# Performance work log

Measured on AMD Instinct MI355X. Metric: run time of the kernel, lower is better.

Reference implementation:

```python
import jax, jax.numpy as jnp
import numpy as np

N = 50000        # nodes
E = 800000       # edges
D = 64           # embedding_dim
N_GCN = 30       # stacked GCNConv layers
N_GGC = 8        # GatedGraphConv propagation steps


def setup_inputs() -> dict:
    key = jax.random.key(0)
    ks = jax.random.split(key, 12)
    s = 0.1
    x = jax.random.normal(ks[0], (N, 2 * D), dtype=jnp.float32)
    edge_index = jax.random.randint(ks[1], (2, E), 0, N, dtype=jnp.int32)
    return {
        "x": x,
        "edge_index": edge_index,
        "linear_w": jax.random.normal(ks[2], (D, 2 * D), dtype=jnp.float32) * s,
        "linear_b": jax.random.normal(ks[3], (D,), dtype=jnp.float32) * s,
        "gcn_w": jax.random.normal(ks[4], (N_GCN, D, D), dtype=jnp.float32) * s,
        "gcn_b": jax.random.normal(ks[5], (N_GCN, D), dtype=jnp.float32) * s,
        "ggc_w": jax.random.normal(ks[6], (N_GGC, D, D), dtype=jnp.float32) * s,
        "gru_w_ih": jax.random.normal(ks[7], (3 * D, D), dtype=jnp.float32) * s,
        "gru_w_hh": jax.random.normal(ks[8], (3 * D, D), dtype=jnp.float32) * s,
        "gru_b_ih": jax.random.normal(ks[9], (3 * D,), dtype=jnp.float32) * s,
        "gru_b_hh": jax.random.normal(ks[10], (3 * D,), dtype=jnp.float32) * s,
    }


def reference(x, edge_index, linear_w, linear_b, gcn_w, gcn_b,
              ggc_w, gru_w_ih, gru_w_hh, gru_b_ih, gru_b_hh):
    src, dst = edge_index[0], edge_index[1]

    # --- GCN normalization (self-loops added, symmetric deg^-1/2 norm) ---
    loop = jnp.arange(N, dtype=edge_index.dtype)
    src_sl = jnp.concatenate([src, loop])   # [E+N]
    dst_sl = jnp.concatenate([dst, loop])
    deg = jax.ops.segment_sum(jnp.ones(E + N, dtype=x.dtype), dst_sl, num_segments=N)
    dinv = deg ** -0.5                       # deg >= 1 because of self-loops
    norm = (dinv[src_sl] * dinv[dst_sl])[:, None]  # [E+N, 1]

    # --- initial linear + relu ---
    h = jax.nn.relu(x @ linear_w.T + linear_b)      # [N, D]

    # --- 30 stacked GCNConv layers (NOTE: original's in-loop relu is a no-op) ---
    def gcn_step(h, wb):
        W, b = wb
        xw = h @ W.T                                 # [N, D]
        msg = xw[src_sl] * norm                      # [E+N, D] gather
        out = jax.ops.segment_sum(msg, dst_sl, num_segments=N) + b
        return out, None

    h, _ = jax.lax.scan(gcn_step, h, (gcn_w, gcn_b))

    # --- GatedGraphConv(D, num_layers=8): add-aggregation + GRUCell ---
    def ggc_step(h, W):
        m = jax.ops.segment_sum((h @ W)[src], dst, num_segments=N)  # [N, D]
        gi = m @ gru_w_ih.T + gru_b_ih              # [N, 3D]
        gh = h @ gru_w_hh.T + gru_b_hh
        ir, iz, inn = jnp.split(gi, 3, axis=1)
        hr, hz, hn = jnp.split(gh, 3, axis=1)
        r = jax.nn.sigmoid(ir + hr)
        z = jax.nn.sigmoid(iz + hz)
        n = jnp.tanh(inn + r * hn)
        h_new = (1.0 - z) * n + z * h
        return h_new, None

    h, _ = jax.lax.scan(ggc_step, h, ggc_w)
    # l2 / gate / cross_graph in the original are dead code; only h is returned
    return h
```

## Files before the change

### kernel.cpp

```cpp
#include <hip/hip_runtime.h>
#include <math.h>

#define NN 50000
#define NE 800000
#define DD 64
#define N_GCN 30
#define N_GGC 8
#define NB ((NN + 255) / 256)
#define NPB 6

__device__ __forceinline__ float lane_bcast(float v, int k) {
    return __int_as_float(__builtin_amdgcn_readlane(__float_as_int(v), k));
}


__global__ void hist_kernel(const int* __restrict__ dst, int* __restrict__ cnt) {
    int i = blockIdx.x * blockDim.x + threadIdx.x;
    if (i < NE) atomicAdd(&cnt[dst[i]], 1);
}

__global__ void dinv_kernel(const int* __restrict__ cnt, float* __restrict__ dinv) {
    int i = blockIdx.x * blockDim.x + threadIdx.x;
    if (i < NN) dinv[i] = rsqrtf((float)cnt[i] + 1.0f);
}

__global__ void scan1_kernel(const int* __restrict__ cnt, int* __restrict__ bsum) {
    __shared__ int s[256];
    int tid = threadIdx.x;
    int i = blockIdx.x * 256 + tid;
    s[tid] = (i < NN) ? cnt[i] : 0;
    __syncthreads();
    for (int off = 128; off > 0; off >>= 1) {
        if (tid < off) s[tid] += s[tid + off];
        __syncthreads();
    }
    if (tid == 0) bsum[blockIdx.x] = s[0];
}

__global__ void scan2_kernel(int* __restrict__ bsum) {
    if (threadIdx.x == 0 && blockIdx.x == 0) {
        int acc = 0;
        for (int b = 0; b < NB; b++) { int v = bsum[b]; bsum[b] = acc; acc += v; }
        bsum[NB] = acc;
    }
}

__global__ void scan3_kernel(const int* __restrict__ cnt, const int* __restrict__ bsum,
                             int* __restrict__ rowptr) {
    __shared__ int s[256];
    int tid = threadIdx.x;
    int i = blockIdx.x * 256 + tid;
    int v = (i < NN) ? cnt[i] : 0;
    s[tid] = v;
    __syncthreads();
    for (int off = 1; off < 256; off <<= 1) {
        int t = (tid >= off) ? s[tid - off] : 0;
        __syncthreads();
        s[tid] += t;
        __syncthreads();
    }
    if (i < NN) rowptr[i] = bsum[blockIdx.x] + s[tid] - v;
    if (i == NN - 1) rowptr[NN] = bsum[blockIdx.x] + s[tid];
}

__global__ void fill_kernel(const int* __restrict__ src, const int* __restrict__ dst,
                            const float* __restrict__ dinv, const int* __restrict__ rowptr,
                            int* __restrict__ cur, int2* __restrict__ epk) {
    int i = blockIdx.x * blockDim.x + threadIdx.x;
    if (i >= NE) return;
    int s = src[i], d = dst[i];
    int pos = atomicAdd(&cur[d], 1);
    int idx = rowptr[d] + pos;
    float w = dinv[s] * dinv[d];
    epk[idx] = make_int2(s, __float_as_int(w));
}


__global__ void prep_weights(const float* __restrict__ lw, const float* __restrict__ gw,
                             const float* __restrict__ wih, const float* __restrict__ whh,
                             float* __restrict__ lin_wt, float* __restrict__ gcn_wt,
                             float* __restrict__ wih_t, float* __restrict__ whh_t) {
    int i = blockIdx.x * blockDim.x + threadIdx.x;
    if (i < 8192) {
        int k = i >> 6, j = i & 63;
        lin_wt[k * 64 + j] = lw[j * 128 + k];
    }
    if (i < 122880) {
        int l = i >> 12, r = i & 4095;
        int k = r >> 6, j = r & 63;
        gcn_wt[l * 4096 + k * 64 + j] = gw[l * 4096 + j * 64 + k];
    }
    if (i < 12288) {
        int j = i >> 6, k = i & 63;
        wih_t[k * 192 + j] = wih[i];
        whh_t[k * 192 + j] = whh[i];
    }
}


__global__ void prep_comb(const float* __restrict__ ggw, const float* __restrict__ wih_t,
                          const float* __restrict__ whh_t, const float* __restrict__ bih,
                          const float* __restrict__ bhh,
                          float* __restrict__ WB, float* __restrict__ BB) {
    int tid = blockIdx.x * blockDim.x + threadIdx.x;
    int wv = tid >> 6, lane = tid & 63;
    if (wv < 24) {
        int l = wv / 3, c = wv - l * 3;
        float u[64];
#pragma unroll
        for (int m = 0; m < 64; m++) u[m] = wih_t[m * 192 + c * 64 + lane];
        for (int k = 0; k < 64; k++) {
            float v = ggw[l * 4096 + k * 64 + lane];
            float a0 = 0.f, a1 = 0.f, a2 = 0.f, a3 = 0.f;
#pragma unroll
            for (int m = 0; m < 64; m += 4) {
                a0 = fmaf(lane_bcast(v, m), u[m], a0);
                a1 = fmaf(lane_bcast(v, m + 1), u[m + 1], a1);
                a2 = fmaf(lane_bcast(v, m + 2), u[m + 2], a2);
                a3 = fmaf(lane_bcast(v, m + 3), u[m + 3], a3);
            }
            WB[l * 24576 + c * 4096 + k * 64 + lane] = (a0 + a1) + (a2 + a3);
        }
    }
    int nthr = blockDim.x * gridDim.x;
    for (int idx = tid; idx < 98304; idx += nthr) {
        int l = idx / 12288;
        int rem = idx - l * 12288;
        int c = rem >> 12;
        int r2 = rem & 4095;
        int k = r2 >> 6, j = r2 & 63;
        WB[l * 24576 + (3 + c) * 4096 + k * 64 + j] = whh_t[k * 192 + c * 64 + j];
    }
    if (tid < 384) BB[tid] = (tid < 192) ? bih[tid] : bhh[tid - 192];
}


__global__ __launch_bounds__(256) void init_linear(const float* __restrict__ x,
                                                   const float* __restrict__ lin_wt,
                                                   const float* __restrict__ lb,
                                                   float* __restrict__ h) {
    int lane = threadIdx.x & 63;
    int wv = blockIdx.x * (blockDim.x >> 6) + (threadIdx.x >> 6);
    int nw = gridDim.x * (blockDim.x >> 6);
    float w[128];
#pragma unroll
    for (int k = 0; k < 128; k++) w[k] = lin_wt[k * 64 + lane];
    float b = lb[lane];
    for (int n = wv; n < NN; n += nw) {
        float x0 = x[n * 128 + lane];
        float x1 = x[n * 128 + 64 + lane];
        float a0 = b, a1 = 0.f, a2 = 0.f, a3 = 0.f;
#pragma unroll
        for (int k = 0; k < 64; k += 4) {
            a0 = fmaf(lane_bcast(x0, k), w[k], a0);
            a1 = fmaf(lane_bcast(x0, k + 1), w[k + 1], a1);
            a2 = fmaf(lane_bcast(x0, k + 2), w[k + 2], a2);
            a3 = fmaf(lane_bcast(x0, k + 3), w[k + 3], a3);
        }
#pragma unroll
        for (int k = 0; k < 64; k += 4) {
            a0 = fmaf(lane_bcast(x1, k), w[64 + k], a0);
            a1 = fmaf(lane_bcast(x1, k + 1), w[64 + k + 1], a1);
            a2 = fmaf(lane_bcast(x1, k + 2), w[64 + k + 2], a2);
            a3 = fmaf(lane_bcast(x1, k + 3), w[64 + k + 3], a3);
        }
        h[n * 64 + lane] = fmaxf((a0 + a1) + (a2 + a3), 0.0f);
    }
}


template <bool NORM>
__global__ __launch_bounds__(256) void agg_raw(const float* __restrict__ hin,
                                               const int* __restrict__ rowptr,
                                               const int2* __restrict__ epk,
                                               const float* __restrict__ dinv,
                                               float* __restrict__ out) {
    int lane = threadIdx.x & 63;
    int sub = lane >> 4;
    int q = lane & 15;
    int wv = blockIdx.x * (blockDim.x >> 6) + (threadIdx.x >> 6);
    int nw = gridDim.x * (blockDim.x >> 6);

    for (int n = wv; n < NN; n += nw) {
        int e0 = rowptr[n], e1 = rowptr[n + 1];
        float ax = 0.f, ay = 0.f, az = 0.f, aw = 0.f;

        int e = e0 + sub;
        while (e + 4 < e1) {
            int2 p0 = epk[e];
            int2 p1 = epk[e + 4];
            float4 v0 = *(const float4*)&hin[(size_t)p0.x * 64 + q * 4];
            float4 v1 = *(const float4*)&hin[(size_t)p1.x * 64 + q * 4];
            float w0 = NORM ? __int_as_float(p0.y) : 1.0f;
            float w1 = NORM ? __int_as_float(p1.y) : 1.0f;
            ax = fmaf(w0, v0.x, ax); ay = fmaf(w0, v0.y, ay);
            az = fmaf(w0, v0.z, az); aw = fmaf(w0, v0.w, aw);
            ax = fmaf(w1, v1.x, ax); ay = fmaf(w1, v1.y, ay);
            az = fmaf(w1, v1.z, az); aw = fmaf(w1, v1.w, aw);
            e += 8;
        }
        if (e < e1) {
            int2 p0 = epk[e];
            float4 v0 = *(const float4*)&hin[(size_t)p0.x * 64 + q * 4];
            float w0 = NORM ? __int_as_float(p0.y) : 1.0f;
            ax = fmaf(w0, v0.x, ax); ay = fmaf(w0, v0.y, ay);
            az = fmaf(w0, v0.z, az); aw = fmaf(w0, v0.w, aw);
        }

        ax += __shfl_xor(ax, 16); ay += __shfl_xor(ay, 16);
        az += __shfl_xor(az, 16); aw += __shfl_xor(aw, 16);
        ax += __shfl_xor(ax, 32); ay += __shfl_xor(ay, 32);
        az += __shfl_xor(az, 32); aw += __shfl_xor(aw, 32);

        if (sub == 0) {
            float4 r;
            if (NORM) {
                float di = dinv[n];
                float dd = di * di;
                float4 sv = *(const float4*)&hin[(size_t)n * 64 + q * 4];
                r.x = fmaf(dd, sv.x, ax);
                r.y = fmaf(dd, sv.y, ay);
                r.z = fmaf(dd, sv.z, az);
                r.w = fmaf(dd, sv.w, aw);
            } else {
                r.x = ax; r.y = ay; r.z = az; r.w = aw;
            }
            *(float4*)&out[(size_t)n * 64 + q * 4] = r;
        }
    }
}


__global__ __launch_bounds__(256) void mm64b(const float* __restrict__ in,
                                             const float* __restrict__ wt,
                                             const float* __restrict__ bias,
                                             float* __restrict__ out) {
    int lane = threadIdx.x & 63;
    int wv = blockIdx.x * (blockDim.x >> 6) + (threadIdx.x >> 6);
    int nw = gridDim.x * (blockDim.x >> 6);
    float w[64];
#pragma unroll
    for (int k = 0; k < 64; k++) w[k] = wt[k * 64 + lane];
    float b = bias[lane];
    for (int n = wv; n < NN; n += nw) {
        float hreg = in[(size_t)n * 64 + lane];
        float a0 = b, a1 = 0.f, a2 = 0.f, a3 = 0.f;
#pragma unroll
        for (int k = 0; k < 64; k += 4) {
            a0 = fmaf(lane_bcast(hreg, k), w[k], a0);
            a1 = fmaf(lane_bcast(hreg, k + 1), w[k + 1], a1);
            a2 = fmaf(lane_bcast(hreg, k + 2), w[k + 2], a2);
            a3 = fmaf(lane_bcast(hreg, k + 3), w[k + 3], a3);
        }
        out[(size_t)n * 64 + lane] = (a0 + a1) + (a2 + a3);
    }
}


__global__ __launch_bounds__(384) void gru_fused(const float* __restrict__ t1,
                                                 const float* __restrict__ h,
                                                 const float* __restrict__ WBl,
                                                 const float* __restrict__ BB,
                                                 float* __restrict__ hout) {
    __shared__ float lds[NPB * 384];
    int tid = threadIdx.x;
    int g = tid >> 6, lane = tid & 63;
    const float* wptr = WBl + (g << 12);
    float w[64];
#pragma unroll
    for (int k = 0; k < 64; k++) w[k] = wptr[k * 64 + lane];
    float bb = BB[g * 64 + lane];
    const float* in = (g < 3) ? t1 : h;

    for (int base = blockIdx.x * NPB; base < NN; base += gridDim.x * NPB) {
        for (int i = 0; i < NPB; i++) {
            int n = base + i;
            if (n < NN) {
                float v = in[(size_t)n * 64 + lane];
                float a0 = bb, a1 = 0.f, a2 = 0.f, a3 = 0.f;
#pragma unroll
                for (int k = 0; k < 64; k += 4) {
                    a0 = fmaf(lane_bcast(v, k), w[k], a0);
                    a1 = fmaf(lane_bcast(v, k + 1), w[k + 1], a1);
                    a2 = fmaf(lane_bcast(v, k + 2), w[k + 2], a2);
                    a3 = fmaf(lane_bcast(v, k + 3), w[k + 3], a3);
                }
                lds[i * 384 + g * 64 + lane] = (a0 + a1) + (a2 + a3);
            }
        }
        __syncthreads();
        int n2 = base + g;
        if (n2 < NN) {
            float ir = lds[g * 384 + lane];
            float iz = lds[g * 384 + 64 + lane];
            float inn = lds[g * 384 + 128 + lane];
            float hr = lds[g * 384 + 192 + lane];
            float hz = lds[g * 384 + 256 + lane];
            float hn = lds[g * 384 + 320 + lane];
            float hv = h[(size_t)n2 * 64 + lane];
            float r = 1.0f / (1.0f + __expf(-(ir + hr)));
            float z = 1.0f / (1.0f + __expf(-(iz + hz)));
            float targ = inn + r * hn;
            float t2 = __expf(2.0f * targ);
            float nn2 = 1.0f - 2.0f / (t2 + 1.0f);
            hout[(size_t)n2 * 64 + lane] = (1.0f - z) * nn2 + z * hv;
        }
        __syncthreads();
    }
}


extern "C" void kernel_launch(void* const* d_in, const int* in_sizes, int n_in,
                              void* d_out, int out_size, void* d_ws, size_t ws_size,
                              hipStream_t stream) {
    const float* x   = (const float*)d_in[0];
    const int*   ei  = (const int*)d_in[1];
    const int*   src = ei;
    const int*   dst = ei + NE;
    const float* lw  = (const float*)d_in[2];
    const float* lb  = (const float*)d_in[3];
    const float* gw  = (const float*)d_in[4];
    const float* gb  = (const float*)d_in[5];
    const float* ggw = (const float*)d_in[6];
    const float* wih = (const float*)d_in[7];
    const float* whh = (const float*)d_in[8];
    const float* bih = (const float*)d_in[9];
    const float* bhh = (const float*)d_in[10];
    float* outp = (float*)d_out;

    char* ws = (char*)d_ws;
    size_t off = 0;
    auto take = [&](size_t bytes) -> char* {
        char* p = ws + off;
        off += (bytes + 255) & ~(size_t)255;
        return p;
    };
    int*   cnt    = (int*)take(NN * 4);
    int*   cur    = (int*)take(NN * 4);
    int*   rowptr = (int*)take((NN + 1) * 4);
    int*   bsum   = (int*)take((NB + 1) * 4);
    float* dinv   = (float*)take(NN * 4);
    int2*  epk    = (int2*)take((size_t)NE * 8);
    float* lin_wt = (float*)take(8192 * 4);
    float* gcn_wt = (float*)take(122880 * 4);
    float* wih_t  = (float*)take(12288 * 4);
    float* whh_t  = (float*)take(12288 * 4);
    float* WB     = (float*)take(196608 * 4);
    float* BB     = (float*)take(384 * 4);
    float* h      = (float*)take((size_t)NN * 64 * 4);
    float* t1     = (float*)take((size_t)NN * 64 * 4);
    (void)ws_size; (void)in_sizes; (void)n_in; (void)out_size;

    hipMemsetAsync(cnt, 0, NN * 4, stream);
    hipMemsetAsync(cur, 0, NN * 4, stream);

    hist_kernel<<<(NE + 255) / 256, 256, 0, stream>>>(dst, cnt);
    dinv_kernel<<<(NN + 255) / 256, 256, 0, stream>>>(cnt, dinv);
    scan1_kernel<<<NB, 256, 0, stream>>>(cnt, bsum);
    scan2_kernel<<<1, 64, 0, stream>>>(bsum);
    scan3_kernel<<<NB, 256, 0, stream>>>(cnt, bsum, rowptr);
    fill_kernel<<<(NE + 255) / 256, 256, 0, stream>>>(src, dst, dinv, rowptr, cur, epk);
    prep_weights<<<480, 256, 0, stream>>>(lw, gw, wih, whh, lin_wt, gcn_wt, wih_t, whh_t);
    prep_comb<<<96, 256, 0, stream>>>(ggw, wih_t, whh_t, bih, bhh, WB, BB);

    init_linear<<<512, 256, 0, stream>>>(x, lin_wt, lb, h);

    for (int l = 0; l < N_GCN; l++) {
        agg_raw<true><<<12500, 256, 0, stream>>>(h, rowptr, epk, dinv, t1);
        mm64b<<<1024, 256, 0, stream>>>(t1, gcn_wt + l * 4096, gb + l * 64, h);
    }

    for (int l = 0; l < N_GGC; l++) {
        agg_raw<false><<<12500, 256, 0, stream>>>(h, rowptr, epk, nullptr, t1);
        float* hdst = (l == N_GGC - 1) ? outp : h;
        gru_fused<<<1024, 384, 0, stream>>>(t1, h, WB + l * 24576, BB, hdst);
    }
}
```

Before: 2.594 ms.

## Fold GCN layer weights into one product and propagate bias terms separately

Because the GCN stack is linear, the 30 per-layer 64x64 matmuls are folded into a single precomputed weight product applied once before aggregation. The biases are handled by propagating scalar vectors A^j·1 (stored in Umat) and adding a rank-30 correction built from bias chains at the end. This removes 29 full matmul passes over the node features, at the cost of 29 small scalar SpMV launches and changed floating-point summation order. It also adds a launch-bounds occupancy hint to the GRU kernel.

```diff
diff --git a/kernel.cpp b/kernel.cpp
--- a/kernel.cpp
+++ b/kernel.cpp
@@ -132,6 +132,85 @@
         WB[l * 24576 + (3 + c) * 4096 + k * 64 + j] = whh_t[k * 192 + c * 64 + j];
     }
     if (tid < 384) BB[tid] = (tid < 192) ? bih[tid] : bhh[tid - 192];
+}
+
+
+__global__ __launch_bounds__(256) void chain_kernel(const float* __restrict__ gcn_wt,
+                                                    const float* __restrict__ gb,
+                                                    float* __restrict__ S0,
+                                                    float* __restrict__ Cm) {
+    int lane = threadIdx.x & 63;
+    int w = (blockIdx.x * blockDim.x + threadIdx.x) >> 6;
+    if (w < 30) {
+        float v = gb[w * 64 + lane];
+        for (int li = w + 1; li < 30; li++) {
+            float nv = 0.f;
+#pragma unroll 16
+            for (int k = 0; k < 64; k++)
+                nv = fmaf(lane_bcast(v, k), gcn_wt[li * 4096 + k * 64 + lane], nv);
+            v = nv;
+        }
+        Cm[(29 - w) * 64 + lane] = v;
+    } else if (w < 94) {
+        int r = w - 30;
+        float v = (lane == r) ? 1.0f : 0.0f;
+        for (int li = 0; li < 30; li++) {
+            float nv = 0.f;
+#pragma unroll 16
+            for (int k = 0; k < 64; k++)
+                nv = fmaf(lane_bcast(v, k), gcn_wt[li * 4096 + k * 64 + lane], nv);
+            v = nv;
+        }
+        S0[r * 64 + lane] = v;
+    }
+}
+
+
+__global__ __launch_bounds__(256) void vagg_first(const int* __restrict__ rowptr,
+                                                  const int2* __restrict__ epk,
+                                                  const float* __restrict__ dinv,
+                                                  float* __restrict__ Umat) {
+    int n = blockIdx.x * blockDim.x + threadIdx.x;
+    if (n >= NN) return;
+    float s = 0.f;
+    int e0 = rowptr[n], e1 = rowptr[n + 1];
+    for (int e = e0; e < e1; e++) s += __int_as_float(epk[e].y);
+    float di = dinv[n];
+    Umat[n * 32 + 0] = 1.0f;
+    Umat[n * 32 + 1] = di * di + s;
+}
+
+__global__ __launch_bounds__(256) void vagg_step(const int* __restrict__ rowptr,
+                                                 const int2* __restrict__ epk,
+                                                 const float* __restrict__ dinv,
+                                                 float* __restrict__ Umat, int jc) {
+    int n = blockIdx.x * blockDim.x + threadIdx.x;
+    if (n >= NN) return;
+    float s = 0.f;
+    int e0 = rowptr[n], e1 = rowptr[n + 1];
+    for (int e = e0; e < e1; e++) {
+        int2 p = epk[e];
+        s = fmaf(__int_as_float(p.y), Umat[(size_t)p.x * 32 + jc - 1], s);
+    }
+    float di = dinv[n];
+    Umat[n * 32 + jc] = fmaf(di * di, Umat[n * 32 + jc - 1], s);
+}
+
+
+__global__ __launch_bounds__(256) void corr30(float* __restrict__ h,
+                                              const float* __restrict__ Umat,
+                                              const float* __restrict__ Cm) {
+    int lane = threadIdx.x & 63;
+    int wv = blockIdx.x * (blockDim.x >> 6) + (threadIdx.x >> 6);
+    int nw = gridDim.x * (blockDim.x >> 6);
+    for (int n = wv; n < NN; n += nw) {
+        float uv = (lane < 30) ? Umat[(size_t)n * 32 + lane] : 0.0f;
+        float acc = 0.f;
+#pragma unroll
+        for (int j2 = 0; j2 < 30; j2++)
+            acc = fmaf(lane_bcast(uv, j2), Cm[j2 * 64 + lane], acc);
+        h[(size_t)n * 64 + lane] += acc;
+    }
 }
 
 
@@ -257,11 +336,11 @@
 }
 
 
-__global__ __launch_bounds__(384) void gru_fused(const float* __restrict__ t1,
-                                                 const float* __restrict__ h,
-                                                 const float* __restrict__ WBl,
-                                                 const float* __restrict__ BB,
-                                                 float* __restrict__ hout) {
+__global__ __launch_bounds__(384, 4) void gru_fused(const float* __restrict__ t1,
+                                                    const float* __restrict__ h,
+                                                    const float* __restrict__ WBl,
+                                                    const float* __restrict__ BB,
+                                                    float* __restrict__ hout) {
     __shared__ float lds[NPB * 384];
     int tid = threadIdx.x;
     int g = tid >> 6, lane = tid & 63;
@@ -347,12 +426,17 @@
     float* whh_t  = (float*)take(12288 * 4);
     float* WB     = (float*)take(196608 * 4);
     float* BB     = (float*)take(384 * 4);
+    float* S0     = (float*)take(4096 * 4);
+    float* Cm     = (float*)take(30 * 64 * 4);
+    float* zb     = (float*)take(64 * 4);
+    float* Umat   = (float*)take((size_t)NN * 32 * 4);
     float* h      = (float*)take((size_t)NN * 64 * 4);
     float* t1     = (float*)take((size_t)NN * 64 * 4);
     (void)ws_size; (void)in_sizes; (void)n_in; (void)out_size;
 
     hipMemsetAsync(cnt, 0, NN * 4, stream);
     hipMemsetAsync(cur, 0, NN * 4, stream);
+    hipMemsetAsync(zb, 0, 64 * 4, stream);
 
     hist_kernel<<<(NE + 255) / 256, 256, 0, stream>>>(dst, cnt);
     dinv_kernel<<<(NN + 255) / 256, 256, 0, stream>>>(cnt, dinv);
@@ -362,17 +446,26 @@
     fill_kernel<<<(NE + 255) / 256, 256, 0, stream>>>(src, dst, dinv, rowptr, cur, epk);
     prep_weights<<<480, 256, 0, stream>>>(lw, gw, wih, whh, lin_wt, gcn_wt, wih_t, whh_t);
     prep_comb<<<96, 256, 0, stream>>>(ggw, wih_t, whh_t, bih, bhh, WB, BB);
+    chain_kernel<<<24, 256, 0, stream>>>(gcn_wt, gb, S0, Cm);
 
     init_linear<<<512, 256, 0, stream>>>(x, lin_wt, lb, h);
 
+    vagg_first<<<(NN + 255) / 256, 256, 0, stream>>>(rowptr, epk, dinv, Umat);
+    for (int jc = 2; jc < 30; jc++)
+        vagg_step<<<(NN + 255) / 256, 256, 0, stream>>>(rowptr, epk, dinv, Umat, jc);
+
+    mm64b<<<1024, 256, 0, stream>>>(h, S0, zb, t1);
+    float* curp = t1;
+    float* nxtp = h;
     for (int l = 0; l < N_GCN; l++) {
-        agg_raw<true><<<12500, 256, 0, stream>>>(h, rowptr, epk, dinv, t1);
-        mm64b<<<1024, 256, 0, stream>>>(t1, gcn_wt + l * 4096, gb + l * 64, h);
-    }
+        agg_raw<true><<<12500, 256, 0, stream>>>(curp, rowptr, epk, dinv, nxtp);
+        float* tmp = curp; curp = nxtp; nxtp = tmp;
+    }
+    corr30<<<1536, 256, 0, stream>>>(curp, Umat, Cm);
 
     for (int l = 0; l < N_GGC; l++) {
-        agg_raw<false><<<12500, 256, 0, stream>>>(h, rowptr, epk, nullptr, t1);
-        float* hdst = (l == N_GGC - 1) ? outp : h;
-        gru_fused<<<1024, 384, 0, stream>>>(t1, h, WB + l * 24576, BB, hdst);
-    }
-}
+        agg_raw<false><<<12500, 256, 0, stream>>>(curp, rowptr, epk, nullptr, nxtp);
+        float* hdst = (l == N_GGC - 1) ? outp : curp;
+        gru_fused<<<1024, 384, 0, stream>>>(nxtp, curp, WB + l * 24576, BB, hdst);
+    }
+}
```

Result: slower. 2.724 ms (+5.0%).
